# Kernel tuning notes

Hardware: AMD Instinct MI355X
Metric: run time of the kernel (lower is better)

## Reference

```python
import jax, jax.numpy as jnp
import numpy as np

D = 128          # fine voxel grid resolution
N0 = 250000
D_IN, D_BASE, D_OUT = 16, 8, 8
EPS = 1e-5
# (cin, cout) for conv0..conv6, conv7, conv9, conv11
_CH = [(16, 8), (8, 16), (16, 16), (16, 32), (32, 32), (32, 64), (64, 64), (64, 32), (32, 16), (16, 8)]

def _offsets():
    r = np.arange(-1, 2)
    return np.stack(np.meshgrid(r, r, r, indexing='ij'), -1).reshape(-1, 3)  # [27,3]

def _lookup_fn(coords, d):
    keys = (coords[:, 0].astype(np.int64) * d + coords[:, 1]) * d + coords[:, 2]
    order = np.argsort(keys)
    skeys = keys[order]
    def lookup(q):
        valid = ((q >= 0) & (q < d)).all(-1)
        k = (q[:, 0].astype(np.int64) * d + q[:, 1]) * d + q[:, 2]
        pos = np.clip(np.searchsorted(skeys, k), 0, len(skeys) - 1)
        return np.where(valid & (skeys[pos] == k), order[pos], -1).astype(np.int32)
    return lookup

def _nbr_same(coords, d):
    # stride-1 sparse conv: outputs at input coords, neighbors at coord+k
    lk = _lookup_fn(coords, d)
    return np.stack([lk(coords + o) for o in _offsets()], 1)  # [N,27]

def _nbr_down(c_out, c_in, d_in):
    # stride-2 conv: output p gathers inputs at 2p+k
    lk = _lookup_fn(c_in, d_in)
    return np.stack([lk(c_out * 2 + o) for o in _offsets()], 1)

def _nbr_up(c_out, c_in, d_in):
    # transposed stride-2 conv: output q gathers input p=(q-k)/2 where divisible
    lk = _lookup_fn(c_in, d_in)
    cols = []
    for o in _offsets():
        q = c_out - o
        div = (q % 2 == 0).all(-1)
        cols.append(np.where(div, lk(q // 2), -1).astype(np.int32))
    return np.stack(cols, 1)

def setup_inputs():
    rng = np.random.default_rng(0)
    flat = rng.choice(D ** 3, size=N0, replace=False)
    c0 = np.stack([flat // (D * D), (flat // D) % D, flat % D], 1).astype(np.int32)
    c1 = np.unique(c0 // 2, axis=0)
    c2 = np.unique(c1 // 2, axis=0)
    c3 = np.unique(c2 // 2, axis=0)
    inp = {
        'feats': jax.random.normal(jax.random.key(0), (N0, D_IN), jnp.float32),
        'nbr0': jnp.asarray(_nbr_same(c0, D)),
        'nbr_d01': jnp.asarray(_nbr_down(c1, c0, D)),
        'nbr1': jnp.asarray(_nbr_same(c1, D // 2)),
        'nbr_d12': jnp.asarray(_nbr_down(c2, c1, D // 2)),
        'nbr2': jnp.asarray(_nbr_same(c2, D // 4)),
        'nbr_d23': jnp.asarray(_nbr_down(c3, c2, D // 4)),
        'nbr3': jnp.asarray(_nbr_same(c3, D // 8)),
        'nbr_u32': jnp.asarray(_nbr_up(c2, c3, D // 8)),
        'nbr_u21': jnp.asarray(_nbr_up(c1, c2, D // 4)),
        'nbr_u10': jnp.asarray(_nbr_up(c0, c1, D // 2)),
    }
    key = jax.random.key(1)
    for i, (ci, co) in enumerate(_CH):
        key, kw = jax.random.split(key)
        inp['w%d' % i] = jax.random.normal(kw, (27, ci, co), jnp.float32) / np.sqrt(27.0 * ci)
        inp['g%d' % i] = jnp.ones((co,), jnp.float32)
        inp['b%d' % i] = jnp.zeros((co,), jnp.float32)
    inp['lin_w'] = jax.random.normal(jax.random.key(2), (D_OUT, D_BASE), jnp.float32) / np.sqrt(D_BASE)
    return inp

def _sconv_bn_relu(f, nbr, w, g, b):
    # f: [Nin,Cin], nbr: [Nout,27] (-1 = no neighbor), w: [27,Cin,Cout]
    gth = jnp.where((nbr >= 0)[..., None], f[jnp.maximum(nbr, 0)], 0.0)  # [Nout,27,Cin]
    y = jnp.einsum('nkc,kco->no', gth, w)
    mu = y.mean(0)                       # training-mode BatchNorm over active voxels
    var = y.var(0)
    return jax.nn.relu((y - mu) * jax.lax.rsqrt(var + EPS) * g + b)

def reference(feats, nbr0, nbr_d01, nbr1, nbr_d12, nbr2, nbr_d23, nbr3, nbr_u32, nbr_u21, nbr_u10,
              w0, g0, b0, w1, g1, b1, w2, g2, b2, w3, g3, b3, w4, g4, b4,
              w5, g5, b5, w6, g6, b6, w7, g7, b7, w8, g8, b8, w9, g9, b9, lin_w):
    c0f = _sconv_bn_relu(feats, nbr0, w0, g0, b0)
    c2f = _sconv_bn_relu(_sconv_bn_relu(c0f, nbr_d01, w1, g1, b1), nbr1, w2, g2, b2)
    c4f = _sconv_bn_relu(_sconv_bn_relu(c2f, nbr_d12, w3, g3, b3), nbr2, w4, g4, b4)
    x = _sconv_bn_relu(_sconv_bn_relu(c4f, nbr_d23, w5, g5, b5), nbr3, w6, g6, b6)
    x = c4f + _sconv_bn_relu(x, nbr_u32, w7, g7, b7)
    x = c2f + _sconv_bn_relu(x, nbr_u21, w8, g8, b8)
    x = c0f + _sconv_bn_relu(x, nbr_u10, w9, g9, b9)
    return x @ lin_w.T, x
```

## Files before the change

kernel.cpp:

```cpp
#include <hip/hip_runtime.h>

#define EPSV 1e-5f

typedef __attribute__((ext_vector_type(8))) short short8;
typedef __attribute__((ext_vector_type(4))) float float4v;

static inline int cdiv(int a, int b) { return (a + b - 1) / b; }
static inline int imin(int a, int b) { return a < b ? a : b; }

__device__ inline unsigned short f2bf(float x) {
  unsigned u = __float_as_uint(x);
  return (unsigned short)((u + 0x7FFFu + ((u >> 16) & 1u)) >> 16);
}
__device__ inline float bf2f(unsigned short u) {
  return __uint_as_float(((unsigned)u) << 16);
}

#define NBUCKET 64

struct PrepArgs {
  const float* w[10];
  unsigned short* wt[10];
  int ci[10];
  int co[10];
  int wcum[11];
  const float* feats;
  unsigned short* featsb;
  int nfeat4;
  float* stats;
};

__global__ __launch_bounds__(256) void prep_kernel(PrepArgs p, long total) {
  const int nstat4 = 10 * NBUCKET * 128 / 4;
  for (long tid0 = (long)blockIdx.x * 256 + threadIdx.x; tid0 < total;
       tid0 += (long)gridDim.x * 256) {
    long tid = tid0;
    if (tid < nstat4) {
      ((float4*)p.stats)[tid] = make_float4(0.f, 0.f, 0.f, 0.f);
      continue;
    }
    tid -= nstat4;
    if (tid < p.nfeat4) {
      float4 v = ((const float4*)p.feats)[tid];
      ushort4 r;
      r.x = f2bf(v.x); r.y = f2bf(v.y); r.z = f2bf(v.z); r.w = f2bf(v.w);
      ((ushort4*)p.featsb)[tid] = r;
      continue;
    }
    tid -= p.nfeat4;
    if (tid >= p.wcum[10]) continue;
    int i = 0;
    while (tid >= p.wcum[i + 1]) ++i;
    int e = (int)(tid - p.wcum[i]);
    int ci = p.ci[i], co = p.co[i];
    int k = e / (ci * co);
    int r = e - k * (ci * co);
    int o = r / ci;
    int c = r - o * ci;
    p.wt[i][((long)k * co + o) * ci + c] = f2bf(p.w[i][((long)k * ci + c) * co + o]);
  }
}

template<int CI, int CO>
__global__ __launch_bounds__(256) void conv_mfma(
    const unsigned short* __restrict__ f, const int* __restrict__ nbr,
    const unsigned short* __restrict__ wt, unsigned short* __restrict__ y,
    float* __restrict__ stats, int nout, int ntiles) {
  constexpr int NCHUNK = (CI == 8) ? 7 : (CI == 16) ? 14 : (CI == 32) ? 27 : 54;

  const int tid = threadIdx.x;
  const int lane = tid & 63;
  const int wid = tid >> 6;
  const int m = lane & 15;
  const int quad = lane >> 4;
  const int cbase = blockIdx.y * 16;
  const int co = cbase + m;
  const bool cok = co < CO;

  auto tapof = [&](int c) -> int {
    if constexpr (CI == 8) return c * 4 + quad;
    else if constexpr (CI == 16) return c * 2 + (quad >> 1);
    else if constexpr (CI == 32) return c;
    else return c >> 1;
  };
  auto cioof = [&](int c) -> int {
    if constexpr (CI == 8) return 0;
    else if constexpr (CI == 16) return (quad & 1) * 8;
    else if constexpr (CI == 32) return quad * 8;
    else return ((c & 1) << 5) + quad * 8;
  };

  float sum = 0.f, sq = 0.f;

  if constexpr (CI <= 16) {
    short8 Bv[NCHUNK];
#pragma unroll
    for (int c = 0; c < NCHUNK; ++c) {
      int tap = tapof(c);
      short8 bq;
#pragma unroll
      for (int q = 0; q < 8; ++q) bq[q] = 0;
      if (cok && tap < 27) bq = *(const short8*)(wt + ((long)tap * CO + co) * CI + cioof(c));
      Bv[c] = bq;
    }
    for (int tile = blockIdx.x; tile < ntiles; tile += gridDim.x) {
      const int rowb = tile * 64 + wid * 16;
      const int row = rowb + m;
      const bool rok = row < nout;
      int idxs[NCHUNK];
#pragma unroll
      for (int c = 0; c < NCHUNK; ++c) {
        int tap = tapof(c);
        idxs[c] = (rok && tap < 27) ? nbr[(long)row * 27 + tap] : -1;
      }
      short8 A[NCHUNK];
#pragma unroll
      for (int c = 0; c < NCHUNK; ++c) {
        short8 a;
#pragma unroll
        for (int q = 0; q < 8; ++q) a[q] = 0;
        if (idxs[c] >= 0) a = *(const short8*)(f + (long)idxs[c] * CI + cioof(c));
        A[c] = a;
      }
      float4v acc = {0.f, 0.f, 0.f, 0.f};
#pragma unroll
      for (int c = 0; c < NCHUNK; ++c)
        acc = __builtin_amdgcn_mfma_f32_16x16x32_bf16(A[c], Bv[c], acc, 0, 0, 0);
#pragma unroll
      for (int r = 0; r < 4; ++r) {
        float v = acc[r];
        int orow = rowb + quad * 4 + r;
        if (cok && orow < nout) y[(long)orow * CO + co] = f2bf(v);
        sum += v;
        sq = fmaf(v, v, sq);
      }
    }
  } else {
    constexpr int G = 9;
    constexpr int NG = NCHUNK / G;
    for (int tile = blockIdx.x; tile < ntiles; tile += gridDim.x) {
      const int rowb = tile * 64 + wid * 16;
      const int row = rowb + m;
      const bool rok = row < nout;
      int idxs[27];
#pragma unroll
      for (int t = 0; t < 27; ++t)
        idxs[t] = rok ? nbr[(long)row * 27 + t] : -1;

      short8 A[2][G], B[2][G];
      auto load_group = [&](int g, int bi) {
#pragma unroll
        for (int j = 0; j < G; ++j) {
          const int c = g * G + j;
          const int tap = tapof(c);
          short8 a, bq;
#pragma unroll
          for (int q = 0; q < 8; ++q) { a[q] = 0; bq[q] = 0; }
          int idx = idxs[tap];
          if (idx >= 0) a = *(const short8*)(f + (long)idx * CI + cioof(c));
          if (cok) bq = *(const short8*)(wt + ((long)tap * CO + co) * CI + cioof(c));
          A[bi][j] = a; B[bi][j] = bq;
        }
      };
      float4v acc = {0.f, 0.f, 0.f, 0.f};
      load_group(0, 0);
#pragma unroll
      for (int g = 0; g < NG; ++g) {
        const int cur = g & 1;
        if (g + 1 < NG) load_group(g + 1, cur ^ 1);
#pragma unroll
        for (int j = 0; j < G; ++j)
          acc = __builtin_amdgcn_mfma_f32_16x16x32_bf16(A[cur][j], B[cur][j], acc, 0, 0, 0);
      }
#pragma unroll
      for (int r = 0; r < 4; ++r) {
        float v = acc[r];
        int orow = rowb + quad * 4 + r;
        if (cok && orow < nout) y[(long)orow * CO + co] = f2bf(v);
        sum += v;
        sq = fmaf(v, v, sq);
      }
    }
  }

  sum += __shfl_xor(sum, 16); sq += __shfl_xor(sq, 16);
  sum += __shfl_xor(sum, 32); sq += __shfl_xor(sq, 32);
  if (quad == 0 && cok) {
    float* st = stats + ((((unsigned)blockIdx.x * 4 + wid) & (NBUCKET - 1)) << 7);
    atomicAdd(&st[co], sum);
    atomicAdd(&st[64 + co], sq);
  }
}

template<int CO>
__global__ __launch_bounds__(256) void bn_relu_bf16(
    const unsigned short* __restrict__ y, const float* __restrict__ stats,
    const float* __restrict__ g, const float* __restrict__ b,
    const unsigned short* __restrict__ skip, unsigned short* __restrict__ out,
    int nout, float inv_n) {
  __shared__ float sA[CO], sC[CO];
  if ((int)threadIdx.x < CO) {
    int o = threadIdx.x;
    float su = 0.f, sq = 0.f;
#pragma unroll 8
    for (int bk = 0; bk < NBUCKET; ++bk) {
      su += stats[bk * 128 + o];
      sq += stats[bk * 128 + 64 + o];
    }
    float mu = su * inv_n;
    float var = sq * inv_n - mu * mu;
    float a = g[o] * rsqrtf(var + EPSV);
    sA[o] = a;
    sC[o] = fmaf(-mu, a, b[o]);
  }
  __syncthreads();
  long total4 = (long)nout * CO / 4;
  for (long i4 = (long)blockIdx.x * 256 + threadIdx.x; i4 < total4;
       i4 += (long)gridDim.x * 256) {
    int o = (int)((i4 * 4) % CO);
    ushort4 v = ((const ushort4*)y)[i4];
    float vv[4] = {bf2f(v.x), bf2f(v.y), bf2f(v.z), bf2f(v.w)};
    unsigned short rr[4];
#pragma unroll
    for (int j = 0; j < 4; ++j) {
      float x = fmaxf(fmaf(vv[j], sA[o + j], sC[o + j]), 0.f);
      if (skip) x += bf2f(skip[i4 * 4 + j]);
      rr[j] = f2bf(x);
    }
    ushort4 r;
    r.x = rr[0]; r.y = rr[1]; r.z = rr[2]; r.w = rr[3];
    ((ushort4*)out)[i4] = r;
  }
}

__global__ __launch_bounds__(256) void tail_kernel(
    const unsigned short* __restrict__ c0f, const float* __restrict__ st9,
    const float* __restrict__ g9, const float* __restrict__ b9, float inv_n,
    const float* __restrict__ lin_w, const unsigned short* __restrict__ y9,
    float* __restrict__ out0, float* __restrict__ x0, int n0) {
  __shared__ float swl[64];
  __shared__ float sbn[16];
  if (threadIdx.x < 64) swl[threadIdx.x] = lin_w[threadIdx.x];
  if (threadIdx.x < 8) {
    int o = threadIdx.x;
    float su = 0.f, sq = 0.f;
#pragma unroll 8
    for (int bk = 0; bk < NBUCKET; ++bk) {
      su += st9[bk * 128 + o];
      sq += st9[bk * 128 + 64 + o];
    }
    float mu = su * inv_n;
    float var = sq * inv_n - mu * mu;
    float a = g9[o] * rsqrtf(var + EPSV);
    sbn[o] = a;
    sbn[8 + o] = fmaf(-mu, a, b9[o]);
  }
  __syncthreads();
  for (int n = blockIdx.x * 256 + threadIdx.x; n < n0; n += gridDim.x * 256) {
    const ushort4* pr = (const ushort4*)(y9 + (long)n * 8);
    ushort4 r0 = pr[0], r1 = pr[1];
    unsigned short rw[8] = {r0.x, r0.y, r0.z, r0.w, r1.x, r1.y, r1.z, r1.w};
    const ushort4* pc = (const ushort4*)(c0f + (long)n * 8);
    ushort4 c0 = pc[0], c1 = pc[1];
    unsigned short cs[8] = {c0.x, c0.y, c0.z, c0.w, c1.x, c1.y, c1.z, c1.w};
    float xv[8];
#pragma unroll
    for (int c = 0; c < 8; ++c)
      xv[c] = bf2f(cs[c]) + fmaxf(fmaf(bf2f(rw[c]), sbn[c], sbn[8 + c]), 0.f);
    *(float4*)(x0 + (long)n * 8) = make_float4(xv[0], xv[1], xv[2], xv[3]);
    *(float4*)(x0 + (long)n * 8 + 4) = make_float4(xv[4], xv[5], xv[6], xv[7]);
    float ov[8];
#pragma unroll
    for (int j = 0; j < 8; ++j) {
      float s = 0.f;
#pragma unroll
      for (int c = 0; c < 8; ++c) s = fmaf(xv[c], swl[j * 8 + c], s);
      ov[j] = s;
    }
    *(float4*)(out0 + (long)n * 8) = make_float4(ov[0], ov[1], ov[2], ov[3]);
    *(float4*)(out0 + (long)n * 8 + 4) = make_float4(ov[4], ov[5], ov[6], ov[7]);
  }
}

extern "C" void kernel_launch(void* const* d_in, const int* in_sizes, int n_in,
                              void* d_out, int out_size, void* d_ws, size_t ws_size,
                              hipStream_t stream) {
  const float* feats   = (const float*)d_in[0];
  const int* nbr0      = (const int*)d_in[1];
  const int* nbr_d01   = (const int*)d_in[2];
  const int* nbr1      = (const int*)d_in[3];
  const int* nbr_d12   = (const int*)d_in[4];
  const int* nbr2      = (const int*)d_in[5];
  const int* nbr_d23   = (const int*)d_in[6];
  const int* nbr3      = (const int*)d_in[7];
  const int* nbr_u32   = (const int*)d_in[8];
  const int* nbr_u21   = (const int*)d_in[9];
  const int* nbr_u10   = (const int*)d_in[10];
  const float* w[10];
  const float* g[10];
  const float* b[10];
  for (int i = 0; i < 10; ++i) {
    w[i] = (const float*)d_in[11 + 3 * i];
    g[i] = (const float*)d_in[12 + 3 * i];
    b[i] = (const float*)d_in[13 + 3 * i];
  }
  const float* lin_w = (const float*)d_in[41];

  const int N0 = in_sizes[0] / 16;
  const int N1 = in_sizes[2] / 27;
  const int N2 = in_sizes[4] / 27;
  const int N3 = in_sizes[6] / 27;
  const float i0 = 1.f / N0, i1 = 1.f / N1, i2 = 1.f / N2, i3 = 1.f / N3;

  static const int CIv[10] = {16, 8, 16, 16, 32, 32, 64, 64, 32, 16};
  static const int COv[10] = {8, 16, 16, 32, 32, 64, 64, 32, 16, 8};

  float* stats = (float*)d_ws;
  unsigned short* u = (unsigned short*)(stats + 10 * NBUCKET * 128);

  unsigned short* yraw = u; u += (size_t)N1 * 32;

  unsigned short* wt[10];
  int wcum[11];
  wcum[0] = 0;
  for (int i = 0; i < 10; ++i) {
    wt[i] = u;
    int sz = 27 * CIv[i] * COv[i];
    u += sz;
    wcum[i + 1] = wcum[i] + sz;
  }
  unsigned short* featsb = u; u += (size_t)N0 * 16;
  unsigned short* c0f = u;    u += (size_t)N0 * 8;
  unsigned short* t1  = u;    u += (size_t)N1 * 16;
  unsigned short* c2f = u;    u += (size_t)N1 * 16;
  unsigned short* t2  = u;    u += (size_t)N2 * 32;
  unsigned short* c4f = u;    u += (size_t)N2 * 32;
  unsigned short* t3  = u;    u += (size_t)N3 * 64;
  unsigned short* t4  = u;    u += (size_t)N3 * 64;
  unsigned short* t5  = t2;
  unsigned short* t6  = t1;
  float* out0 = (float*)d_out;
  float* x0   = (float*)d_out + (size_t)N0 * 8;

  float* s[10];
  for (int i = 0; i < 10; ++i) s[i] = stats + i * NBUCKET * 128;

  PrepArgs pa;
  for (int i = 0; i < 10; ++i) {
    pa.w[i] = w[i]; pa.wt[i] = wt[i];
    pa.ci[i] = CIv[i]; pa.co[i] = COv[i];
    pa.wcum[i] = wcum[i];
  }
  pa.wcum[10] = wcum[10];
  pa.feats = feats; pa.featsb = featsb;
  pa.nfeat4 = N0 * 16 / 4;
  pa.stats = stats;
  long prep_total = (10 * NBUCKET * 128 / 4) + pa.nfeat4 + wcum[10];
  prep_kernel<<<imin((int)((prep_total + 255) / 256), 2048), 256, 0, stream>>>(pa, prep_total);

  auto bgrid = [](long nout, int co) {
    return imin((int)((nout * co / 4 + 255) / 256), 1024);
  };
  auto cgrid = [](int ntiles) { return imin(ntiles, 1024); };

  int tb0 = cdiv(N0, 64), tb1 = cdiv(N1, 64), tb2 = cdiv(N2, 64), tb3 = cdiv(N3, 64);

  conv_mfma<16, 8><<<dim3(cgrid(tb0), 1), 256, 0, stream>>>(featsb, nbr0, wt[0], yraw, s[0], N0, tb0);
  bn_relu_bf16<8><<<bgrid(N0, 8), 256, 0, stream>>>(yraw, s[0], g[0], b[0], nullptr, c0f, N0, i0);

  conv_mfma<8, 16><<<dim3(cgrid(tb1), 1), 256, 0, stream>>>(c0f, nbr_d01, wt[1], yraw, s[1], N1, tb1);
  bn_relu_bf16<16><<<bgrid(N1, 16), 256, 0, stream>>>(yraw, s[1], g[1], b[1], nullptr, t1, N1, i1);

  conv_mfma<16, 16><<<dim3(cgrid(tb1), 1), 256, 0, stream>>>(t1, nbr1, wt[2], yraw, s[2], N1, tb1);
  bn_relu_bf16<16><<<bgrid(N1, 16), 256, 0, stream>>>(yraw, s[2], g[2], b[2], nullptr, c2f, N1, i1);

  conv_mfma<16, 32><<<dim3(cgrid(tb2), 2), 256, 0, stream>>>(c2f, nbr_d12, wt[3], yraw, s[3], N2, tb2);
  bn_relu_bf16<32><<<bgrid(N2, 32), 256, 0, stream>>>(yraw, s[3], g[3], b[3], nullptr, t2, N2, i2);

  conv_mfma<32, 32><<<dim3(cgrid(tb2), 2), 256, 0, stream>>>(t2, nbr2, wt[4], yraw, s[4], N2, tb2);
  bn_relu_bf16<32><<<bgrid(N2, 32), 256, 0, stream>>>(yraw, s[4], g[4], b[4], nullptr, c4f, N2, i2);

  conv_mfma<32, 64><<<dim3(cgrid(tb3), 4), 256, 0, stream>>>(c4f, nbr_d23, wt[5], yraw, s[5], N3, tb3);
  bn_relu_bf16<64><<<bgrid(N3, 64), 256, 0, stream>>>(yraw, s[5], g[5], b[5], nullptr, t3, N3, i3);

  conv_mfma<64, 64><<<dim3(cgrid(tb3), 4), 256, 0, stream>>>(t3, nbr3, wt[6], yraw, s[6], N3, tb3);
  bn_relu_bf16<64><<<bgrid(N3, 64), 256, 0, stream>>>(yraw, s[6], g[6], b[6], nullptr, t4, N3, i3);

  conv_mfma<64, 32><<<dim3(cgrid(tb2), 2), 256, 0, stream>>>(t4, nbr_u32, wt[7], yraw, s[7], N2, tb2);
  bn_relu_bf16<32><<<bgrid(N2, 32), 256, 0, stream>>>(yraw, s[7], g[7], b[7], c4f, t5, N2, i2);

  conv_mfma<32, 16><<<dim3(cgrid(tb1), 1), 256, 0, stream>>>(t5, nbr_u21, wt[8], yraw, s[8], N1, tb1);
  bn_relu_bf16<16><<<bgrid(N1, 16), 256, 0, stream>>>(yraw, s[8], g[8], b[8], c2f, t6, N1, i1);

  conv_mfma<16, 8><<<dim3(cgrid(tb0), 1), 256, 0, stream>>>(t6, nbr_u10, wt[9], yraw, s[9], N0, tb0);

  tail_kernel<<<imin(cdiv(N0, 256), 1024), 256, 0, stream>>>(
      c0f, s[9], g[9], b[9], i0, lin_w, yraw, out0, x0, N0);
}
```

Before: 480.0 us.

## Stage neighbor indices in LDS, skip empty taps, pre-swizzle weights per lane

Each wave now loads its 16x27 neighbor-index block with coalesced reads into shared memory instead of each lane doing strided loads. A wave-wide ballot then marks chunks where no row has a valid neighbor, and both the gathers and the MFMAs for those chunks are skipped, which matters at this sparsity. For CI>=32 the weights are pre-swizzled during prep into a per-lane MFMA fragment layout so each lane does one contiguous 16-byte load. The cost is extra LDS traffic, ballot overhead and divergent control flow around the MFMA chain.

```diff
diff --git a/kernel.cpp b/kernel.cpp
--- a/kernel.cpp
+++ b/kernel.cpp
@@ -57,16 +57,28 @@
     int r = e - k * (ci * co);
     int o = r / ci;
     int c = r - o * ci;
-    p.wt[i][((long)k * co + o) * ci + c] = f2bf(p.w[i][((long)k * ci + c) * co + o]);
+    float val = p.w[i][((long)k * ci + c) * co + o];
+    if (ci >= 32) {
+      int chunk, quad, j;
+      if (ci == 32) { chunk = k; quad = c >> 3; j = c & 7; }
+      else { chunk = k * 2 + (c >> 5); int rem = c & 31; quad = rem >> 3; j = rem & 7; }
+      int lane_ = quad * 16 + (o & 15);
+      int cb = o >> 4;
+      long dst = (((long)chunk * (co >> 4) + cb) * 64 + lane_) * 8 + j;
+      p.wt[i][dst] = f2bf(val);
+    } else {
+      p.wt[i][((long)k * co + o) * ci + c] = f2bf(val);
+    }
   }
 }
 
 template<int CI, int CO>
 __global__ __launch_bounds__(256) void conv_mfma(
     const unsigned short* __restrict__ f, const int* __restrict__ nbr,
-    const unsigned short* __restrict__ wt, unsigned short* __restrict__ y,
+    const unsigned short* __restrict__ wtd, unsigned short* __restrict__ y,
     float* __restrict__ stats, int nout, int ntiles) {
   constexpr int NCHUNK = (CI == 8) ? 7 : (CI == 16) ? 14 : (CI == 32) ? 27 : 54;
+  __shared__ int sIdx[4 * 448];
 
   const int tid = threadIdx.x;
   const int lane = tid & 63;
@@ -76,6 +88,7 @@
   const int cbase = blockIdx.y * 16;
   const int co = cbase + m;
   const bool cok = co < CO;
+  int* myIdx = &sIdx[wid * 448];
 
   auto tapof = [&](int c) -> int {
     if constexpr (CI == 8) return c * 4 + quad;
@@ -100,18 +113,33 @@
       short8 bq;
 #pragma unroll
       for (int q = 0; q < 8; ++q) bq[q] = 0;
-      if (cok && tap < 27) bq = *(const short8*)(wt + ((long)tap * CO + co) * CI + cioof(c));
+      if (cok && tap < 27)
+        bq = *(const short8*)(wtd + ((long)tap * CO + co) * CI + cioof(c));
       Bv[c] = bq;
     }
     for (int tile = blockIdx.x; tile < ntiles; tile += gridDim.x) {
       const int rowb = tile * 64 + wid * 16;
-      const int row = rowb + m;
-      const bool rok = row < nout;
+      {
+        const int* src = nbr + (long)rowb * 27;
+#pragma unroll
+        for (int j = 0; j < 7; ++j) {
+          int off = j * 64 + lane;
+          int v = -1;
+          if (off < 432) {
+            int r = off / 27;
+            if (rowb + r < nout) v = src[off];
+          }
+          myIdx[off] = v;
+        }
+      }
+      unsigned actm = 0;
       int idxs[NCHUNK];
 #pragma unroll
       for (int c = 0; c < NCHUNK; ++c) {
         int tap = tapof(c);
-        idxs[c] = (rok && tap < 27) ? nbr[(long)row * 27 + tap] : -1;
+        int idx = (tap < 27) ? myIdx[m * 27 + tap] : -1;
+        idxs[c] = idx;
+        if (__ballot(idx >= 0) != 0ull) actm |= 1u << c;
       }
       short8 A[NCHUNK];
 #pragma unroll
@@ -119,17 +147,20 @@
         short8 a;
 #pragma unroll
         for (int q = 0; q < 8; ++q) a[q] = 0;
-        if (idxs[c] >= 0) a = *(const short8*)(f + (long)idxs[c] * CI + cioof(c));
+        if ((actm >> c) & 1) {
+          if (idxs[c] >= 0) a = *(const short8*)(f + (long)idxs[c] * CI + cioof(c));
+        }
         A[c] = a;
       }
       float4v acc = {0.f, 0.f, 0.f, 0.f};
 #pragma unroll
       for (int c = 0; c < NCHUNK; ++c)
-        acc = __builtin_amdgcn_mfma_f32_16x16x32_bf16(A[c], Bv[c], acc, 0, 0, 0);
+        if ((actm >> c) & 1)
+          acc = __builtin_amdgcn_mfma_f32_16x16x32_bf16(A[c], Bv[c], acc, 0, 0, 0);
 #pragma unroll
       for (int r = 0; r < 4; ++r) {
         float v = acc[r];
-        int orow = rowb + quad * 4 + r;
+        int orow = tile * 64 + wid * 16 + quad * 4 + r;
         if (cok && orow < nout) y[(long)orow * CO + co] = f2bf(v);
         sum += v;
         sq = fmaf(v, v, sq);
@@ -140,26 +171,39 @@
     constexpr int NG = NCHUNK / G;
     for (int tile = blockIdx.x; tile < ntiles; tile += gridDim.x) {
       const int rowb = tile * 64 + wid * 16;
-      const int row = rowb + m;
-      const bool rok = row < nout;
-      int idxs[27];
-#pragma unroll
-      for (int t = 0; t < 27; ++t)
-        idxs[t] = rok ? nbr[(long)row * 27 + t] : -1;
-
+      {
+        const int* src = nbr + (long)rowb * 27;
+#pragma unroll
+        for (int j = 0; j < 7; ++j) {
+          int off = j * 64 + lane;
+          int v = -1;
+          if (off < 432) {
+            int r = off / 27;
+            if (rowb + r < nout) v = src[off];
+          }
+          myIdx[off] = v;
+        }
+      }
+      unsigned long long actm = 0;
+#pragma unroll
+      for (int c = 0; c < NCHUNK; ++c) {
+        int idx = myIdx[m * 27 + tapof(c)];
+        if (__ballot(idx >= 0) != 0ull) actm |= 1ull << c;
+      }
       short8 A[2][G], B[2][G];
       auto load_group = [&](int g, int bi) {
 #pragma unroll
-        for (int j = 0; j < G; ++j) {
-          const int c = g * G + j;
-          const int tap = tapof(c);
+        for (int j2 = 0; j2 < G; ++j2) {
+          const int c = g * G + j2;
           short8 a, bq;
 #pragma unroll
           for (int q = 0; q < 8; ++q) { a[q] = 0; bq[q] = 0; }
-          int idx = idxs[tap];
-          if (idx >= 0) a = *(const short8*)(f + (long)idx * CI + cioof(c));
-          if (cok) bq = *(const short8*)(wt + ((long)tap * CO + co) * CI + cioof(c));
-          A[bi][j] = a; B[bi][j] = bq;
+          if ((actm >> c) & 1) {
+            int idx = myIdx[m * 27 + tapof(c)];
+            if (idx >= 0) a = *(const short8*)(f + (long)idx * CI + cioof(c));
+            bq = *(const short8*)(wtd + (((long)c * (CO / 16) + blockIdx.y) * 64 + lane) * 8);
+          }
+          A[bi][j2] = a; B[bi][j2] = bq;
         }
       };
       float4v acc = {0.f, 0.f, 0.f, 0.f};
@@ -169,14 +213,15 @@
         const int cur = g & 1;
         if (g + 1 < NG) load_group(g + 1, cur ^ 1);
 #pragma unroll
-        for (int j = 0; j < G; ++j)
-          acc = __builtin_amdgcn_mfma_f32_16x16x32_bf16(A[cur][j], B[cur][j], acc, 0, 0, 0);
+        for (int j2 = 0; j2 < G; ++j2)
+          if ((actm >> (g * G + j2)) & 1)
+            acc = __builtin_amdgcn_mfma_f32_16x16x32_bf16(A[cur][j2], B[cur][j2], acc, 0, 0, 0);
       }
 #pragma unroll
       for (int r = 0; r < 4; ++r) {
         float v = acc[r];
-        int orow = rowb + quad * 4 + r;
-        if (cok && orow < nout) y[(long)orow * CO + co] = f2bf(v);
+        int orow = tile * 64 + wid * 16 + quad * 4 + r;
+        if (orow < nout) y[(long)orow * CO + co] = f2bf(v);
         sum += v;
         sq = fmaf(v, v, sq);
       }
```

Measured after the change: 520.8 us. 8.5% more time.

## Stage wide-input conv weights in LDS and skip MFMAs for empty neighbor taps

Applied to the files above, without the earlier changes.

For convs with 32 or more input channels, the weight prep now writes weights in a fragment-major layout. Each block copies its output-column weight slice into shared memory once and reads B fragments from LDS, instead of reloading them from global memory on every tile. For narrow-input convs, a wave-wide ballot marks chunks where no row has a valid neighbor, and both the gather and the MFMA are skipped for those chunks. In exchange this uses more LDS, which may reduce occupancy, and adds ballot overhead; with sparse inputs, entirely empty chunks across 16 rows are likely rare.

```diff
diff --git a/kernel.cpp b/kernel.cpp
--- a/kernel.cpp
+++ b/kernel.cpp
@@ -57,16 +57,29 @@
     int r = e - k * (ci * co);
     int o = r / ci;
     int c = r - o * ci;
-    p.wt[i][((long)k * co + o) * ci + c] = f2bf(p.w[i][((long)k * ci + c) * co + o]);
+    float val = p.w[i][((long)k * ci + c) * co + o];
+    if (ci >= 32) {
+      int chunk, quad, j;
+      if (ci == 32) { chunk = k; quad = c >> 3; j = c & 7; }
+      else { chunk = k * 2 + (c >> 5); int rem = c & 31; quad = rem >> 3; j = rem & 7; }
+      int lane_ = quad * 16 + (o & 15);
+      int cb = o >> 4;
+      long dst = (((long)chunk * (co >> 4) + cb) * 64 + lane_) * 8 + j;
+      p.wt[i][dst] = f2bf(val);
+    } else {
+      p.wt[i][((long)k * co + o) * ci + c] = f2bf(val);
+    }
   }
 }
 
 template<int CI, int CO>
 __global__ __launch_bounds__(256) void conv_mfma(
     const unsigned short* __restrict__ f, const int* __restrict__ nbr,
-    const unsigned short* __restrict__ wt, unsigned short* __restrict__ y,
+    const unsigned short* __restrict__ wtd, unsigned short* __restrict__ y,
     float* __restrict__ stats, int nout, int ntiles) {
   constexpr int NCHUNK = (CI == 8) ? 7 : (CI == 16) ? 14 : (CI == 32) ? 27 : 54;
+  constexpr int SBSZ = (CI >= 32) ? NCHUNK * 512 : 8;
+  __shared__ short sB[SBSZ];
 
   const int tid = threadIdx.x;
   const int lane = tid & 63;
@@ -100,18 +113,22 @@
       short8 bq;
 #pragma unroll
       for (int q = 0; q < 8; ++q) bq[q] = 0;
-      if (cok && tap < 27) bq = *(const short8*)(wt + ((long)tap * CO + co) * CI + cioof(c));
+      if (cok && tap < 27)
+        bq = *(const short8*)(wtd + ((long)tap * CO + co) * CI + cioof(c));
       Bv[c] = bq;
     }
     for (int tile = blockIdx.x; tile < ntiles; tile += gridDim.x) {
       const int rowb = tile * 64 + wid * 16;
       const int row = rowb + m;
       const bool rok = row < nout;
+      unsigned actm = 0;
       int idxs[NCHUNK];
 #pragma unroll
       for (int c = 0; c < NCHUNK; ++c) {
         int tap = tapof(c);
-        idxs[c] = (rok && tap < 27) ? nbr[(long)row * 27 + tap] : -1;
+        int idx = (rok && tap < 27) ? nbr[(long)row * 27 + tap] : -1;
+        idxs[c] = idx;
+        if (__ballot(idx >= 0) != 0ull) actm |= 1u << c;
       }
       short8 A[NCHUNK];
 #pragma unroll
@@ -119,13 +136,16 @@
         short8 a;
 #pragma unroll
         for (int q = 0; q < 8; ++q) a[q] = 0;
-        if (idxs[c] >= 0) a = *(const short8*)(f + (long)idxs[c] * CI + cioof(c));
+        if ((actm >> c) & 1) {
+          if (idxs[c] >= 0) a = *(const short8*)(f + (long)idxs[c] * CI + cioof(c));
+        }
         A[c] = a;
       }
       float4v acc = {0.f, 0.f, 0.f, 0.f};
 #pragma unroll
       for (int c = 0; c < NCHUNK; ++c)
-        acc = __builtin_amdgcn_mfma_f32_16x16x32_bf16(A[c], Bv[c], acc, 0, 0, 0);
+        if ((actm >> c) & 1)
+          acc = __builtin_amdgcn_mfma_f32_16x16x32_bf16(A[c], Bv[c], acc, 0, 0, 0);
 #pragma unroll
       for (int r = 0; r < 4; ++r) {
         float v = acc[r];
@@ -136,6 +156,16 @@
       }
     }
   } else {
+    {
+      const int nfrag = NCHUNK * 64;
+      for (int i = tid; i < nfrag; i += 256) {
+        int c = i >> 6;
+        int l = i & 63;
+        *(short8*)(sB + (long)i * 8) =
+            *(const short8*)(wtd + (((long)c * (CO / 16) + blockIdx.y) * 64 + l) * 8);
+      }
+      __syncthreads();
+    }
     constexpr int G = 9;
     constexpr int NG = NCHUNK / G;
     for (int tile = blockIdx.x; tile < ntiles; tile += gridDim.x) {
@@ -147,19 +177,17 @@
       for (int t = 0; t < 27; ++t)
         idxs[t] = rok ? nbr[(long)row * 27 + t] : -1;
 
-      short8 A[2][G], B[2][G];
+      short8 A[2][G];
       auto load_group = [&](int g, int bi) {
 #pragma unroll
-        for (int j = 0; j < G; ++j) {
-          const int c = g * G + j;
-          const int tap = tapof(c);
-          short8 a, bq;
-#pragma unroll
-          for (int q = 0; q < 8; ++q) { a[q] = 0; bq[q] = 0; }
-          int idx = idxs[tap];
+        for (int j2 = 0; j2 < G; ++j2) {
+          const int c = g * G + j2;
+          short8 a;
+#pragma unroll
+          for (int q = 0; q < 8; ++q) a[q] = 0;
+          int idx = idxs[tapof(c)];
           if (idx >= 0) a = *(const short8*)(f + (long)idx * CI + cioof(c));
-          if (cok) bq = *(const short8*)(wt + ((long)tap * CO + co) * CI + cioof(c));
-          A[bi][j] = a; B[bi][j] = bq;
+          A[bi][j2] = a;
         }
       };
       float4v acc = {0.f, 0.f, 0.f, 0.f};
@@ -169,14 +197,17 @@
         const int cur = g & 1;
         if (g + 1 < NG) load_group(g + 1, cur ^ 1);
 #pragma unroll
-        for (int j = 0; j < G; ++j)
-          acc = __builtin_amdgcn_mfma_f32_16x16x32_bf16(A[cur][j], B[cur][j], acc, 0, 0, 0);
+        for (int j2 = 0; j2 < G; ++j2) {
+          const int c = g * G + j2;
+          short8 bq = *(const short8*)(sB + ((long)c * 64 + lane) * 8);
+          acc = __builtin_amdgcn_mfma_f32_16x16x32_bf16(A[cur][j2], bq, acc, 0, 0, 0);
+        }
       }
 #pragma unroll
       for (int r = 0; r < 4; ++r) {
         float v = acc[r];
         int orow = rowb + quad * 4 + r;
-        if (cok && orow < nout) y[(long)orow * CO + co] = f2bf(v);
+        if (orow < nout) y[(long)orow * CO + co] = f2bf(v);
         sum += v;
         sq = fmaf(v, v, sq);
       }
```

Result: slower. 506.8 us (+5.6%).
